# Optimization experiments

Hardware: AMD Instinct MI355X
Metric: run time of the kernel (lower is better)

## Reference

```python
import jax, jax.numpy as jnp
import numpy as np

C = 1.0          # ball curvature (k = -1/c with c=1.0 in the torch module)
SQC = 1.0        # sqrt(C)
LN_EPS = 1e-5

def _artanh(x):
    return jnp.arctanh(jnp.clip(x, -1.0 + 1e-7, 1.0 - 1e-7))

def _norm(x):
    # last-dim L2 norm, clamped away from zero for stable division
    return jnp.clip(jnp.sqrt(jnp.sum(x * x, axis=-1, keepdims=True)), 1e-7, None)

def expmap0(u):
    un = _norm(u)
    return jnp.tanh(SQC * un) * u / (SQC * un)

def logmap0(y):
    yn = _norm(y)
    return _artanh(SQC * yn) * y / (SQC * yn)

def mobius_add(x, y):
    x2 = jnp.sum(x * x, axis=-1, keepdims=True)
    y2 = jnp.sum(y * y, axis=-1, keepdims=True)
    xy = jnp.sum(x * y, axis=-1, keepdims=True)
    num = (1.0 + 2.0 * C * xy + C * y2) * x + (1.0 - C * x2) * y
    den = 1.0 + 2.0 * C * xy + C * C * x2 * y2
    return num / jnp.clip(den, 1e-15, None)

def mobius_matvec(W, x):
    # W: [H, D], x: [B, D] -> [B, H]
    mx = x @ W.T
    xn = _norm(x)
    mxn = _norm(mx)
    res = jnp.tanh(mxn / xn * _artanh(SQC * xn)) * mx / (SQC * mxn)
    return jnp.where(mxn <= 1e-7, jnp.zeros_like(res), res)

def mobius_pointwise_mul(w, x):
    wx = w * x
    xn = _norm(x)
    wxn = _norm(wx)
    res = jnp.tanh(wxn / xn * _artanh(SQC * xn)) * wx / (SQC * wxn)
    return jnp.where(wxn <= 1e-7, jnp.zeros_like(res), res)

def layer_norm(x, g, b):
    mu = jnp.mean(x, axis=-1, keepdims=True)
    var = jnp.mean((x - mu) ** 2, axis=-1, keepdims=True)
    return (x - mu) * jax.lax.rsqrt(var + LN_EPS) * g + b

def one_rnn_transform(W, h, U, x, b):
    Wh = mobius_matvec(W, h)
    Ux = mobius_matvec(U, x)
    return mobius_add(mobius_add(Wh, Ux), b)

def setup_inputs() -> dict:
    key = jax.random.key(0)
    B, I, H = 65536, 256, 256
    k1, k2, k3, k4, k5 = jax.random.split(key, 5)
    stdv = 1.0 / np.sqrt(H)
    # points on the Poincare ball via expmap0 of small tangent vectors
    x = expmap0(0.02 * jax.random.normal(k1, (B, I), dtype=jnp.float32))
    hx = expmap0(0.02 * jax.random.normal(k2, (B, H), dtype=jnp.float32))
    weight_ih = jax.random.uniform(k3, (3 * H, I), dtype=jnp.float32, minval=-stdv, maxval=stdv)
    weight_hh = jax.random.uniform(k4, (3 * H, H), dtype=jnp.float32, minval=-stdv, maxval=stdv)
    bias = 0.01 * jax.random.normal(k5, (3, H), dtype=jnp.float32)
    ln_gamma = jnp.ones((3, H), dtype=jnp.float32)
    ln_beta = jnp.zeros((3, H), dtype=jnp.float32)
    return {"input": x, "hx": hx, "weight_ih": weight_ih, "weight_hh": weight_hh,
            "bias": bias, "ln_gamma": ln_gamma, "ln_beta": ln_beta}

def reference(input, hx, weight_ih, weight_hh, bias, ln_gamma, ln_beta):
    H = hx.shape[-1]
    W_ir, W_ih_, W_iz = weight_ih[:H], weight_ih[H:2*H], weight_ih[2*H:]
    W_hr, W_hh_, W_hz = weight_hh[:H], weight_hh[H:2*H], weight_hh[2*H:]
    b_r, b_h, b_z = bias[0], bias[1], bias[2]
    temp_z = logmap0(one_rnn_transform(W_hz, hx, W_iz, input, b_z))
    temp_r = logmap0(one_rnn_transform(W_hr, hx, W_ir, input, b_r))
    z_t = jax.nn.sigmoid(layer_norm(temp_z, ln_gamma[0], ln_beta[0]))
    r_t = jax.nn.sigmoid(layer_norm(temp_r, ln_gamma[1], ln_beta[1]))
    rh_t = mobius_pointwise_mul(r_t, hx)
    h_tilde = one_rnn_transform(W_hh_, rh_t, W_ih_, input, b_h)
    h_tilde = expmap0(jnp.tanh(layer_norm(logmap0(h_tilde), ln_gamma[2], ln_beta[2])))
    temp_1 = mobius_pointwise_mul(1.0 - z_t, hx)
    temp_2 = mobius_pointwise_mul(z_t, h_tilde)
    return mobius_add(temp_1, temp_2)
```

## Files before the change

kernel.cpp:

```cpp
#include <hip/hip_runtime.h>
#include <math.h>

#define HD  256
#define BM  16
#define NTH 256

typedef __attribute__((ext_vector_type(8))) short bf16x8;
typedef __attribute__((ext_vector_type(4))) float f32x4;

__device__ __forceinline__ float rcp_f(float x){ return __builtin_amdgcn_rcpf(x); }
__device__ __forceinline__ float tanh_f(float x){
  float ax = fabsf(x);
  float e  = __expf(-2.f*ax);
  float t  = (1.f - e) * rcp_f(1.f + e);
  return copysignf(t, x);
}
__device__ __forceinline__ float artanh_f(float v){
  v = fminf(fmaxf(v, -1.f + 1e-7f), 1.f - 1e-7f);
  return 0.5f * __logf((1.f + v) * rcp_f(1.f - v));
}
__device__ __forceinline__ float sigmoid_f(float v){ return rcp_f(1.f + __expf(-v)); }
__device__ __forceinline__ unsigned short f2bf(float f){
  unsigned u = __float_as_uint(f);
  u += 0x7FFFu + ((u >> 16) & 1u);
  return (unsigned short)(u >> 16);
}
__device__ __forceinline__ float bf2f(unsigned short h){
  return __uint_as_float(((unsigned)h) << 16);
}
__device__ __forceinline__ int swz(int R, int C){
  return R*HD + (((C >> 3) ^ (R & 7)) << 3) + (C & 7);
}

__global__ void convert_w_kernel(const float* __restrict__ Wih,
                                 const float* __restrict__ Whh,
                                 unsigned short* __restrict__ wb){
  int c = blockIdx.x * blockDim.x + threadIdx.x;
  if (c >= 6 * 8192) return;
  int mat = c >> 13;
  int ci  = c & 8191;
  int l = ci & 63, st = ci >> 6;
  int s = st & 7, ct = st >> 3;
  int col = ct * 16 + (l & 15);
  int k0  = s * 32 + (l >> 4) * 8;
  const float* src = (mat < 3) ? (Wih + (size_t)mat * HD * HD)
                               : (Whh + (size_t)(mat - 3) * HD * HD);
  const float* p = src + (size_t)col * HD + k0;
  unsigned short tmp[8];
  #pragma unroll
  for (int j = 0; j < 8; ++j) tmp[j] = f2bf(p[j]);
  *(bf16x8*)(wb + (size_t)mat * 65536 + (size_t)ci * 8) = *(bf16x8*)tmp;
}

__device__ __forceinline__ void gate_gemm(
    const unsigned short* ldsH, const unsigned short* __restrict__ wH,
    const unsigned short* ldsX, const unsigned short* __restrict__ wX,
    f32x4 A[4], f32x4 Bx[4], int wc, int lr, int lg, int l){
  #pragma unroll
  for (int n = 0; n < 4; ++n){
    A[n]  = (f32x4){0.f,0.f,0.f,0.f};
    Bx[n] = (f32x4){0.f,0.f,0.f,0.f};
  }
  #pragma unroll
  for (int s = 0; s < 8; ++s){
    int idx = lr*HD + (((4*s + lg) ^ (lr & 7)) << 3);
    bf16x8 ah = *(const bf16x8*)&ldsH[idx];
    bf16x8 ax = *(const bf16x8*)&ldsX[idx];
    #pragma unroll
    for (int n = 0; n < 4; ++n){
      int ct = wc*4 + n;
      int off = ((ct*8 + s)*64 + l)*8;
      bf16x8 bh = *(const bf16x8*)(wH + off);
      bf16x8 bx = *(const bf16x8*)(wX + off);
      A[n]  = __builtin_amdgcn_mfma_f32_16x16x32_bf16(ah, bh, A[n], 0, 0, 0);
      Bx[n] = __builtin_amdgcn_mfma_f32_16x16x32_bf16(ax, bx, Bx[n], 0, 0, 0);
    }
  }
}

__device__ __forceinline__ void gate_reduce_chain(
    const f32x4 (&A)[4], const f32x4 (&Bx)[4], const float (&bt)[4],
    float (*RED)[33], float (*kco)[9], float (*srow)[BM], const float* sbb,
    int rowA, int gidx, int t, int wc, int lr, int lg){
  float p[7][4];
  #pragma unroll
  for (int q = 0; q < 4; ++q){
    float a2=0.f,b2=0.f,ab=0.f,sA=0.f,sB=0.f,Ab=0.f,Bb=0.f;
    #pragma unroll
    for (int n = 0; n < 4; ++n){
      float ae = A[n][q], be = Bx[n][q], bv = bt[n];
      a2 = fmaf(ae,ae,a2); b2 = fmaf(be,be,b2); ab = fmaf(ae,be,ab);
      sA += ae; sB += be; Ab = fmaf(ae,bv,Ab); Bb = fmaf(be,bv,Bb);
    }
    p[0][q]=a2; p[1][q]=b2; p[2][q]=ab; p[3][q]=sA; p[4][q]=sB; p[5][q]=Ab; p[6][q]=Bb;
  }
  #pragma unroll
  for (int j = 0; j < 7; ++j)
    #pragma unroll
    for (int q = 0; q < 4; ++q){
      float v = p[j][q];
      v += __shfl_xor(v,1); v += __shfl_xor(v,2);
      v += __shfl_xor(v,4); v += __shfl_xor(v,8);
      p[j][q] = v;
    }
  if (lr == 0){
    #pragma unroll
    for (int q = 0; q < 4; ++q){
      int R = lg*4 + q;
      #pragma unroll
      for (int j = 0; j < 7; ++j) RED[R][wc*8 + j] = p[j][q];
    }
  }
  __syncthreads();
  if (t < BM){
    int R = t;
    float s[7];
    #pragma unroll
    for (int j = 0; j < 7; ++j)
      s[j] = RED[R][j] + RED[R][8+j] + RED[R][16+j] + RED[R][24+j];
    float bb  = sbb[gidx];
    float sbs = sbb[4+gidx];
    float an = srow[rowA][R], aa = srow[rowA+1][R];
    float bn = srow[0][R],    ba = srow[1][R];
    float mraw = sqrtf(s[0]); float mA = fmaxf(mraw, 1e-7f);
    float tA = tanh_f(mA / an * aa);
    float sa  = (mraw <= 1e-7f) ? 0.f : tA / mA;
    float x2a = (mraw <= 1e-7f) ? 0.f : tA*tA;
    float nraw = sqrtf(s[1]); float mB = fmaxf(nraw, 1e-7f);
    float tB = tanh_f(mB / bn * ba);
    float sb_ = (nraw <= 1e-7f) ? 0.f : tB / mB;
    float x2b = (nraw <= 1e-7f) ? 0.f : tB*tB;
    float xy = sa*sb_*s[2];
    float ca = 1.f + 2.f*xy + x2b;
    float cb = 1.f - x2a;
    float den = fmaxf(1.f + 2.f*xy + x2a*x2b, 1e-15f);
    float u = ca*sa/den, v = cb*sb_/den;
    float P2 = u*u*s[0] + 2.f*u*v*s[2] + v*v*s[1];
    float Pb = u*s[5] + v*s[6];
    float sP = u*s[3] + v*s[4];
    float ca2 = 1.f + 2.f*Pb + bb;
    float cb2 = 1.f - P2;
    float den2 = fmaxf(1.f + 2.f*Pb + P2*bb, 1e-15f);
    float pp = ca2/den2, ww = cb2/den2;
    float Q2 = pp*pp*P2 + 2.f*pp*ww*Pb + ww*ww*bb;
    float sQsum = pp*sP + ww*sbs;
    float qn = fmaxf(sqrtf(Q2), 1e-7f);
    float sQ = artanh_f(qn) / qn;
    float mu = sQ*sQsum*(1.f/HD);
    float e2 = sQ*sQ*Q2*(1.f/HD);
    float is = rsqrtf(e2 - mu*mu + 1e-5f);
    kco[R][0] = sQ*pp*u;  kco[R][1] = sQ*pp*v;  kco[R][2] = sQ*ww;
    kco[R][3] = mu;       kco[R][4] = is;
  }
  __syncthreads();
}

__global__ __launch_bounds__(NTH, 2) void mobius_gru_mfma(
    const float* __restrict__ x, const float* __restrict__ hx,
    const unsigned short* __restrict__ wbih, const unsigned short* __restrict__ wbhh,
    const float* __restrict__ bias, const float* __restrict__ gam,
    const float* __restrict__ bet, float* __restrict__ out, int B){
  __shared__ unsigned short xb[BM*HD];
  __shared__ unsigned short hb[BM*HD];
  __shared__ float RED[BM][33];
  __shared__ float kco[BM][9];
  __shared__ float srow[8][BM];
  __shared__ float sbb[8];

  const int t  = threadIdx.x;
  const int l  = t & 63;
  const int lr = l & 15, lg = l >> 4;
  const int wc = t >> 6;
  const size_t row0 = (size_t)blockIdx.x * BM;

  {
    float* spart = &RED[0][0];
    int r = t >> 4, seg = t & 15;
    const float* xp = x  + (row0 + r)*HD + seg*16;
    const float* hp = hx + (row0 + r)*HD + seg*16;
    float sx = 0.f, sh = 0.f;
    #pragma unroll
    for (int i = 0; i < 4; ++i){
      int c = seg*16 + i*4;
      int di = swz(r, c);
      float4 v = *(const float4*)(xp + i*4);
      sx += v.x*v.x + v.y*v.y + v.z*v.z + v.w*v.w;
      ushort4 o = { f2bf(v.x), f2bf(v.y), f2bf(v.z), f2bf(v.w) };
      *(ushort4*)&xb[di] = o;
      v = *(const float4*)(hp + i*4);
      sh += v.x*v.x + v.y*v.y + v.z*v.z + v.w*v.w;
      ushort4 o2 = { f2bf(v.x), f2bf(v.y), f2bf(v.z), f2bf(v.w) };
      *(ushort4*)&hb[di] = o2;
    }
    spart[r*16 + seg] = sx; spart[256 + r*16 + seg] = sh;
  }
  if (t >= 64 && t < 256){
    int g = (t >> 6) - 1;
    float4 b4 = *(const float4*)&bias[g*HD + (t & 63)*4];
    float p2 = b4.x*b4.x + b4.y*b4.y + b4.z*b4.z + b4.w*b4.w;
    float ps = b4.x + b4.y + b4.z + b4.w;
    #pragma unroll
    for (int m = 1; m <= 32; m <<= 1){ p2 += __shfl_xor(p2, m); ps += __shfl_xor(ps, m); }
    if ((t & 63) == 0){ sbb[g] = p2; sbb[4+g] = ps; }
  }
  __syncthreads();
  if (t < BM){
    float* spart = &RED[0][0];
    float sx = 0.f, sh = 0.f;
    #pragma unroll
    for (int i = 0; i < 16; ++i){ sx += spart[t*16 + i]; sh += spart[256 + t*16 + i]; }
    float xn = fmaxf(sqrtf(sx), 1e-7f);
    float hn = fmaxf(sqrtf(sh), 1e-7f);
    srow[0][t] = xn; srow[1][t] = artanh_f(xn);
    srow[2][t] = hn; srow[3][t] = artanh_f(hn);
  }
  __syncthreads();

  f32x4 A[4], Bx[4];
  float bt[4], gv[4], bv[4];
  unsigned ztp[4][2];
  float hvreg[4][4];

  #pragma unroll
  for (int n = 0; n < 4; ++n){
    int C = wc*64 + n*16 + lr;
    bt[n] = bias[2*HD + C]; gv[n] = gam[C]; bv[n] = bet[C];
  }
  gate_gemm(hb, wbhh + 2*65536, xb, wbih + 2*65536, A, Bx, wc, lr, lg, l);
  gate_reduce_chain(A, Bx, bt, RED, kco, srow, sbb, 2, 2, t, wc, lr, lg);
  #pragma unroll
  for (int q = 0; q < 4; ++q){
    int R = lg*4 + q;
    float KA=kco[R][0], KB=kco[R][1], Kb=kco[R][2], mu=kco[R][3], is=kco[R][4];
    #pragma unroll
    for (int n = 0; n < 4; ++n){
      float ln = (KA*A[n][q] + KB*Bx[n][q] + Kb*bt[n] - mu)*is*gv[n] + bv[n];
      unsigned zb = f2bf(sigmoid_f(ln));
      if ((q & 1) == 0) ztp[n][q>>1] = zb;
      else              ztp[n][q>>1] |= (zb << 16);
    }
  }

  #pragma unroll
  for (int n = 0; n < 4; ++n){
    int C = wc*64 + n*16 + lr;
    bt[n] = bias[C]; gv[n] = gam[HD + C]; bv[n] = bet[HD + C];
  }
  gate_gemm(hb, wbhh, xb, wbih, A, Bx, wc, lr, lg, l);
  gate_reduce_chain(A, Bx, bt, RED, kco, srow, sbb, 2, 0, t, wc, lr, lg);
  {
    #pragma unroll
    for (int q = 0; q < 4; ++q){
      int R = lg*4 + q;
      float KA=kco[R][0], KB=kco[R][1], Kb=kco[R][2], mu=kco[R][3], is=kco[R][4];
      float acc = 0.f;
      #pragma unroll
      for (int n = 0; n < 4; ++n){
        int C = wc*64 + n*16 + lr;
        float hv = bf2f(hb[swz(R, C)]);
        hvreg[n][q] = hv;
        float ln = (KA*A[n][q] + KB*Bx[n][q] + Kb*bt[n] - mu)*is*gv[n] + bv[n];
        float rhv = sigmoid_f(ln) * hv;
        Bx[n][q] = rhv;
        acc = fmaf(rhv, rhv, acc);
      }
      float v2 = acc;
      v2 += __shfl_xor(v2,1); v2 += __shfl_xor(v2,2);
      v2 += __shfl_xor(v2,4); v2 += __shfl_xor(v2,8);
      if (lr == 0) RED[R][wc*8] = v2;
    }
  }
  __syncthreads();
  if (t < BM){
    int R = t;
    float s0 = RED[R][0] + RED[R][8] + RED[R][16] + RED[R][24];
    float wraw = sqrtf(s0); float wn = fmaxf(wraw, 1e-7f);
    float s = tanh_f(wn / srow[2][R] * srow[3][R]);
    float sc = (wraw <= 1e-7f) ? 0.f : s / wn;
    float rn = fmaxf((wraw <= 1e-7f) ? 0.f : fabsf(s), 1e-7f);
    kco[R][0] = sc; srow[4][R] = rn; srow[5][R] = artanh_f(rn);
  }
  __syncthreads();
  #pragma unroll
  for (int q = 0; q < 4; ++q){
    int R = lg*4 + q;
    float sc = kco[R][0];
    #pragma unroll
    for (int n = 0; n < 4; ++n){
      int C = wc*64 + n*16 + lr;
      hb[swz(R, C)] = f2bf(sc * Bx[n][q]);
    }
  }
  __syncthreads();

  #pragma unroll
  for (int n = 0; n < 4; ++n){
    int C = wc*64 + n*16 + lr;
    bt[n] = bias[HD + C]; gv[n] = gam[2*HD + C]; bv[n] = bet[2*HD + C];
  }
  gate_gemm(hb, wbhh + 65536, xb, wbih + 65536, A, Bx, wc, lr, lg, l);
  gate_reduce_chain(A, Bx, bt, RED, kco, srow, sbb, 4, 1, t, wc, lr, lg);
  {
    #pragma unroll
    for (int q = 0; q < 4; ++q){
      int R = lg*4 + q;
      float KA=kco[R][0], KB=kco[R][1], Kb=kco[R][2], mu=kco[R][3], is=kco[R][4];
      float acc = 0.f;
      #pragma unroll
      for (int n = 0; n < 4; ++n){
        float ln = (KA*A[n][q] + KB*Bx[n][q] + Kb*bt[n] - mu)*is*gv[n] + bv[n];
        float uv = tanh_f(ln);
        A[n][q] = uv;
        acc = fmaf(uv, uv, acc);
      }
      float v2 = acc;
      v2 += __shfl_xor(v2,1); v2 += __shfl_xor(v2,2);
      v2 += __shfl_xor(v2,4); v2 += __shfl_xor(v2,8);
      if (lr == 0) RED[R][wc*8] = v2;
    }
  }
  __syncthreads();
  if (t < BM){
    int R = t;
    float s0 = RED[R][0] + RED[R][8] + RED[R][16] + RED[R][24];
    float unraw = sqrtf(s0);
    float un = fmaxf(unraw, 1e-7f);
    float es = tanh_f(un) / un;
    float htn = fmaxf(es * unraw, 1e-7f);
    kco[R][0] = es; srow[6][R] = htn; srow[7][R] = artanh_f(htn);
  }
  __syncthreads();

  #pragma unroll
  for (int q = 0; q < 4; ++q){
    int R = lg*4 + q;
    float es = kco[R][0];
    float a1 = 0.f, a2 = 0.f, a12 = 0.f;
    #pragma unroll
    for (int n = 0; n < 4; ++n){
      unsigned zp = ztp[n][q >> 1];
      float zv = __uint_as_float((q & 1) ? (zp & 0xFFFF0000u) : (zp << 16));
      float w2v = zv * es * A[n][q];
      float w1v = (1.f - zv) * hvreg[n][q];
      A[n][q]  = w1v;
      Bx[n][q] = w2v;
      a1 = fmaf(w1v, w1v, a1); a2 = fmaf(w2v, w2v, a2); a12 = fmaf(w1v, w2v, a12);
    }
    float v1 = a1, v2 = a2, v3 = a12;
    v1 += __shfl_xor(v1,1); v2 += __shfl_xor(v2,1); v3 += __shfl_xor(v3,1);
    v1 += __shfl_xor(v1,2); v2 += __shfl_xor(v2,2); v3 += __shfl_xor(v3,2);
    v1 += __shfl_xor(v1,4); v2 += __shfl_xor(v2,4); v3 += __shfl_xor(v3,4);
    v1 += __shfl_xor(v1,8); v2 += __shfl_xor(v2,8); v3 += __shfl_xor(v3,8);
    if (lr == 0){
      RED[R][wc*8]   = v1;
      RED[R][wc*8+1] = v2;
      RED[R][wc*8+2] = v3;
    }
  }
  __syncthreads();
  if (t < BM){
    int R = t;
    float s1  = RED[R][0] + RED[R][8]  + RED[R][16] + RED[R][24];
    float s2  = RED[R][1] + RED[R][9]  + RED[R][17] + RED[R][25];
    float s12 = RED[R][2] + RED[R][10] + RED[R][18] + RED[R][26];
    float raw1 = sqrtf(s1); float n1 = fmaxf(raw1, 1e-7f);
    float ss1 = tanh_f(n1 / srow[2][R] * srow[3][R]);
    float sc1 = (raw1 <= 1e-7f) ? 0.f : ss1 / n1;
    float t1  = (raw1 <= 1e-7f) ? 0.f : ss1*ss1;
    float raw2 = sqrtf(s2); float n2 = fmaxf(raw2, 1e-7f);
    float ss2 = tanh_f(n2 / srow[6][R] * srow[7][R]);
    float sc2 = (raw2 <= 1e-7f) ? 0.f : ss2 / n2;
    float t2  = (raw2 <= 1e-7f) ? 0.f : ss2*ss2;
    float xy = sc1*sc2*s12;
    float ca = 1.f + 2.f*xy + t2;
    float cb = 1.f - t1;
    float den = fmaxf(1.f + 2.f*xy + t1*t2, 1e-15f);
    kco[R][0] = ca*sc1/den;
    kco[R][1] = cb*sc2/den;
  }
  __syncthreads();
  #pragma unroll
  for (int q = 0; q < 4; ++q){
    int R = lg*4 + q;
    float cw1 = kco[R][0], cw2 = kco[R][1];
    #pragma unroll
    for (int n = 0; n < 4; ++n){
      int C = wc*64 + n*16 + lr;
      out[(row0 + R)*HD + C] = cw1*A[n][q] + cw2*Bx[n][q];
    }
  }
}

extern "C" void kernel_launch(void* const* d_in, const int* in_sizes, int n_in,
                              void* d_out, int out_size, void* d_ws, size_t ws_size,
                              hipStream_t stream){
  const float* x    = (const float*)d_in[0];
  const float* hx   = (const float*)d_in[1];
  const float* Wih  = (const float*)d_in[2];
  const float* Whh  = (const float*)d_in[3];
  const float* bias = (const float*)d_in[4];
  const float* gam  = (const float*)d_in[5];
  const float* bet  = (const float*)d_in[6];
  float* out = (float*)d_out;
  unsigned short* wb = (unsigned short*)d_ws;
  const int B = in_sizes[0] / HD;

  hipLaunchKernelGGL(convert_w_kernel, dim3(192), dim3(256), 0, stream, Wih, Whh, wb);
  hipLaunchKernelGGL(mobius_gru_mfma, dim3(B / BM), dim3(NTH), 0, stream,
                     x, hx, wb, wb + 3*65536, bias, gam, bet, out, B);
}
```

Measured before the change: 222.8 us.

## Process 32 rows per block so each weight fragment feeds two MFMA row groups

Raises the block's row tile from 16 to 32. Each bf16 weight fragment fetched from global memory now feeds two 16-row MFMA accumulator sets, which halves weight traffic per output row. All per-row epilogue loops (reductions, gate math, stores) gain an outer loop over the two row groups, and the input staging is remapped to 8 threads per row. The cost is roughly double the accumulator and per-thread state registers, which may lower occupancy, and half as many blocks in the grid.

```diff
diff --git a/kernel.cpp b/kernel.cpp
--- a/kernel.cpp
+++ b/kernel.cpp
@@ -2,7 +2,7 @@
 #include <math.h>
 
 #define HD  256
-#define BM  16
+#define BM  32
 #define NTH 256
 
 typedef __attribute__((ext_vector_type(8))) short bf16x8;
@@ -55,60 +55,71 @@
 __device__ __forceinline__ void gate_gemm(
     const unsigned short* ldsH, const unsigned short* __restrict__ wH,
     const unsigned short* ldsX, const unsigned short* __restrict__ wX,
-    f32x4 A[4], f32x4 Bx[4], int wc, int lr, int lg, int l){
-  #pragma unroll
-  for (int n = 0; n < 4; ++n){
-    A[n]  = (f32x4){0.f,0.f,0.f,0.f};
-    Bx[n] = (f32x4){0.f,0.f,0.f,0.f};
-  }
+    f32x4 A[2][4], f32x4 Bx[2][4], int wc, int lr, int lg, int l){
+  #pragma unroll
+  for (int g = 0; g < 2; ++g)
+    #pragma unroll
+    for (int n = 0; n < 4; ++n){
+      A[g][n]  = (f32x4){0.f,0.f,0.f,0.f};
+      Bx[g][n] = (f32x4){0.f,0.f,0.f,0.f};
+    }
   #pragma unroll
   for (int s = 0; s < 8; ++s){
-    int idx = lr*HD + (((4*s + lg) ^ (lr & 7)) << 3);
-    bf16x8 ah = *(const bf16x8*)&ldsH[idx];
-    bf16x8 ax = *(const bf16x8*)&ldsX[idx];
+    int col = (((4*s + lg) ^ (lr & 7)) << 3);
+    int i0 = lr*HD + col;
+    int i1 = (lr + 16)*HD + col;
+    bf16x8 ah0 = *(const bf16x8*)&ldsH[i0];
+    bf16x8 ah1 = *(const bf16x8*)&ldsH[i1];
+    bf16x8 ax0 = *(const bf16x8*)&ldsX[i0];
+    bf16x8 ax1 = *(const bf16x8*)&ldsX[i1];
     #pragma unroll
     for (int n = 0; n < 4; ++n){
       int ct = wc*4 + n;
       int off = ((ct*8 + s)*64 + l)*8;
       bf16x8 bh = *(const bf16x8*)(wH + off);
       bf16x8 bx = *(const bf16x8*)(wX + off);
-      A[n]  = __builtin_amdgcn_mfma_f32_16x16x32_bf16(ah, bh, A[n], 0, 0, 0);
-      Bx[n] = __builtin_amdgcn_mfma_f32_16x16x32_bf16(ax, bx, Bx[n], 0, 0, 0);
+      A[0][n]  = __builtin_amdgcn_mfma_f32_16x16x32_bf16(ah0, bh, A[0][n], 0, 0, 0);
+      A[1][n]  = __builtin_amdgcn_mfma_f32_16x16x32_bf16(ah1, bh, A[1][n], 0, 0, 0);
+      Bx[0][n] = __builtin_amdgcn_mfma_f32_16x16x32_bf16(ax0, bx, Bx[0][n], 0, 0, 0);
+      Bx[1][n] = __builtin_amdgcn_mfma_f32_16x16x32_bf16(ax1, bx, Bx[1][n], 0, 0, 0);
     }
   }
 }
 
 __device__ __forceinline__ void gate_reduce_chain(
-    const f32x4 (&A)[4], const f32x4 (&Bx)[4], const float (&bt)[4],
+    const f32x4 (&A)[2][4], const f32x4 (&Bx)[2][4], const float (&bt)[4],
     float (*RED)[33], float (*kco)[9], float (*srow)[BM], const float* sbb,
     int rowA, int gidx, int t, int wc, int lr, int lg){
-  float p[7][4];
-  #pragma unroll
-  for (int q = 0; q < 4; ++q){
-    float a2=0.f,b2=0.f,ab=0.f,sA=0.f,sB=0.f,Ab=0.f,Bb=0.f;
-    #pragma unroll
-    for (int n = 0; n < 4; ++n){
-      float ae = A[n][q], be = Bx[n][q], bv = bt[n];
-      a2 = fmaf(ae,ae,a2); b2 = fmaf(be,be,b2); ab = fmaf(ae,be,ab);
-      sA += ae; sB += be; Ab = fmaf(ae,bv,Ab); Bb = fmaf(be,bv,Bb);
-    }
-    p[0][q]=a2; p[1][q]=b2; p[2][q]=ab; p[3][q]=sA; p[4][q]=sB; p[5][q]=Ab; p[6][q]=Bb;
-  }
-  #pragma unroll
-  for (int j = 0; j < 7; ++j)
+  #pragma unroll
+  for (int g = 0; g < 2; ++g){
+    float p[7][4];
     #pragma unroll
     for (int q = 0; q < 4; ++q){
-      float v = p[j][q];
-      v += __shfl_xor(v,1); v += __shfl_xor(v,2);
-      v += __shfl_xor(v,4); v += __shfl_xor(v,8);
-      p[j][q] = v;
-    }
-  if (lr == 0){
-    #pragma unroll
-    for (int q = 0; q < 4; ++q){
-      int R = lg*4 + q;
-      #pragma unroll
-      for (int j = 0; j < 7; ++j) RED[R][wc*8 + j] = p[j][q];
+      float a2=0.f,b2=0.f,ab=0.f,sA=0.f,sB=0.f,Ab=0.f,Bb=0.f;
+      #pragma unroll
+      for (int n = 0; n < 4; ++n){
+        float ae = A[g][n][q], be = Bx[g][n][q], bv = bt[n];
+        a2 = fmaf(ae,ae,a2); b2 = fmaf(be,be,b2); ab = fmaf(ae,be,ab);
+        sA += ae; sB += be; Ab = fmaf(ae,bv,Ab); Bb = fmaf(be,bv,Bb);
+      }
+      p[0][q]=a2; p[1][q]=b2; p[2][q]=ab; p[3][q]=sA; p[4][q]=sB; p[5][q]=Ab; p[6][q]=Bb;
+    }
+    #pragma unroll
+    for (int j = 0; j < 7; ++j)
+      #pragma unroll
+      for (int q = 0; q < 4; ++q){
+        float v = p[j][q];
+        v += __shfl_xor(v,1); v += __shfl_xor(v,2);
+        v += __shfl_xor(v,4); v += __shfl_xor(v,8);
+        p[j][q] = v;
+      }
+    if (lr == 0){
+      #pragma unroll
+      for (int q = 0; q < 4; ++q){
+        int R = g*16 + lg*4 + q;
+        #pragma unroll
+        for (int j = 0; j < 7; ++j) RED[R][wc*8 + j] = p[j][q];
+      }
     }
   }
   __syncthreads();
@@ -175,13 +186,13 @@
 
   {
     float* spart = &RED[0][0];
-    int r = t >> 4, seg = t & 15;
-    const float* xp = x  + (row0 + r)*HD + seg*16;
-    const float* hp = hx + (row0 + r)*HD + seg*16;
+    int r = t >> 3, seg = t & 7;
+    const float* xp = x  + (row0 + r)*HD + seg*32;
+    const float* hp = hx + (row0 + r)*HD + seg*32;
     float sx = 0.f, sh = 0.f;
     #pragma unroll
-    for (int i = 0; i < 4; ++i){
-      int c = seg*16 + i*4;
+    for (int i = 0; i < 8; ++i){
+      int c = seg*32 + i*4;
       int di = swz(r, c);
       float4 v = *(const float4*)(xp + i*4);
       sx += v.x*v.x + v.y*v.y + v.z*v.z + v.w*v.w;
@@ -192,7 +203,7 @@
       ushort4 o2 = { f2bf(v.x), f2bf(v.y), f2bf(v.z), f2bf(v.w) };
       *(ushort4*)&hb[di] = o2;
     }
-    spart[r*16 + seg] = sx; spart[256 + r*16 + seg] = sh;
+    spart[r*8 + seg] = sx; spart[256 + r*8 + seg] = sh;
   }
   if (t >= 64 && t < 256){
     int g = (t >> 6) - 1;
@@ -208,7 +219,7 @@
     float* spart = &RED[0][0];
     float sx = 0.f, sh = 0.f;
     #pragma unroll
-    for (int i = 0; i < 16; ++i){ sx += spart[t*16 + i]; sh += spart[256 + t*16 + i]; }
+    for (int i = 0; i < 8; ++i){ sx += spart[t*8 + i]; sh += spart[256 + t*8 + i]; }
     float xn = fmaxf(sqrtf(sx), 1e-7f);
     float hn = fmaxf(sqrtf(sh), 1e-7f);
     srow[0][t] = xn; srow[1][t] = artanh_f(xn);
@@ -216,10 +227,10 @@
   }
   __syncthreads();
 
-  f32x4 A[4], Bx[4];
+  f32x4 A[2][4], Bx[2][4];
   float bt[4], gv[4], bv[4];
-  unsigned ztp[4][2];
-  float hvreg[4][4];
+  unsigned ztp[2][4][2];
+  float hvreg[2][4][4];
 
   #pragma unroll
   for (int n = 0; n < 4; ++n){
@@ -229,17 +240,19 @@
   gate_gemm(hb, wbhh + 2*65536, xb, wbih + 2*65536, A, Bx, wc, lr, lg, l);
   gate_reduce_chain(A, Bx, bt, RED, kco, srow, sbb, 2, 2, t, wc, lr, lg);
   #pragma unroll
-  for (int q = 0; q < 4; ++q){
-    int R = lg*4 + q;
-    float KA=kco[R][0], KB=kco[R][1], Kb=kco[R][2], mu=kco[R][3], is=kco[R][4];
-    #pragma unroll
-    for (int n = 0; n < 4; ++n){
-      float ln = (KA*A[n][q] + KB*Bx[n][q] + Kb*bt[n] - mu)*is*gv[n] + bv[n];
-      unsigned zb = f2bf(sigmoid_f(ln));
-      if ((q & 1) == 0) ztp[n][q>>1] = zb;
-      else              ztp[n][q>>1] |= (zb << 16);
-    }
-  }
+  for (int g = 0; g < 2; ++g)
+    #pragma unroll
+    for (int q = 0; q < 4; ++q){
+      int R = g*16 + lg*4 + q;
+      float KA=kco[R][0], KB=kco[R][1], Kb=kco[R][2], mu=kco[R][3], is=kco[R][4];
+      #pragma unroll
+      for (int n = 0; n < 4; ++n){
+        float ln = (KA*A[g][n][q] + KB*Bx[g][n][q] + Kb*bt[n] - mu)*is*gv[n] + bv[n];
+        unsigned zb = f2bf(sigmoid_f(ln));
+        if ((q & 1) == 0) ztp[g][n][q>>1] = zb;
+        else              ztp[g][n][q>>1] |= (zb << 16);
+      }
+    }
 
   #pragma unroll
   for (int n = 0; n < 4; ++n){
@@ -250,25 +263,27 @@
   gate_reduce_chain(A, Bx, bt, RED, kco, srow, sbb, 2, 0, t, wc, lr, lg);
   {
     #pragma unroll
-    for (int q = 0; q < 4; ++q){
-      int R = lg*4 + q;
-      float KA=kco[R][0], KB=kco[R][1], Kb=kco[R][2], mu=kco[R][3], is=kco[R][4];
-      float acc = 0.f;
-      #pragma unroll
-      for (int n = 0; n < 4; ++n){
-        int C = wc*64 + n*16 + lr;
-        float hv = bf2f(hb[swz(R, C)]);
-        hvreg[n][q] = hv;
-        float ln = (KA*A[n][q] + KB*Bx[n][q] + Kb*bt[n] - mu)*is*gv[n] + bv[n];
-        float rhv = sigmoid_f(ln) * hv;
-        Bx[n][q] = rhv;
-        acc = fmaf(rhv, rhv, acc);
-      }
-      float v2 = acc;
-      v2 += __shfl_xor(v2,1); v2 += __shfl_xor(v2,2);
-      v2 += __shfl_xor(v2,4); v2 += __shfl_xor(v2,8);
-      if (lr == 0) RED[R][wc*8] = v2;
-    }
+    for (int g = 0; g < 2; ++g)
+      #pragma unroll
+      for (int q = 0; q < 4; ++q){
+        int R = g*16 + lg*4 + q;
+        float KA=kco[R][0], KB=kco[R][1], Kb=kco[R][2], mu=kco[R][3], is=kco[R][4];
+        float acc = 0.f;
+        #pragma unroll
+        for (int n = 0; n < 4; ++n){
+          int C = wc*64 + n*16 + lr;
+          float hv = bf2f(hb[swz(R, C)]);
+          hvreg[g][n][q] = hv;
+          float ln = (KA*A[g][n][q] + KB*Bx[g][n][q] + Kb*bt[n] - mu)*is*gv[n] + bv[n];
+          float rhv = sigmoid_f(ln) * hv;
+          Bx[g][n][q] = rhv;
+          acc = fmaf(rhv, rhv, acc);
+        }
+        float v2 = acc;
+        v2 += __shfl_xor(v2,1); v2 += __shfl_xor(v2,2);
+        v2 += __shfl_xor(v2,4); v2 += __shfl_xor(v2,8);
+        if (lr == 0) RED[R][wc*8] = v2;
+      }
   }
   __syncthreads();
   if (t < BM){
@@ -282,15 +297,17 @@
   }
   __syncthreads();
   #pragma unroll
-  for (int q = 0; q < 4; ++q){
-    int R = lg*4 + q;
-    float sc = kco[R][0];
-    #pragma unroll
-    for (int n = 0; n < 4; ++n){
-      int C = wc*64 + n*16 + lr;
-      hb[swz(R, C)] = f2bf(sc * Bx[n][q]);
-    }
-  }
+  for (int g = 0; g < 2; ++g)
+    #pragma unroll
+    for (int q = 0; q < 4; ++q){
+      int R = g*16 + lg*4 + q;
+      float sc = kco[R][0];
+      #pragma unroll
+      for (int n = 0; n < 4; ++n){
+        int C = wc*64 + n*16 + lr;
+        hb[swz(R, C)] = f2bf(sc * Bx[g][n][q]);
+      }
+    }
   __syncthreads();
 
   #pragma unroll
@@ -302,22 +319,24 @@
   gate_reduce_chain(A, Bx, bt, RED, kco, srow, sbb, 4, 1, t, wc, lr, lg);
   {
     #pragma unroll
-    for (int q = 0; q < 4; ++q){
-      int R = lg*4 + q;
-      float KA=kco[R][0], KB=kco[R][1], Kb=kco[R][2], mu=kco[R][3], is=kco[R][4];
-      float acc = 0.f;
-      #pragma unroll
-      for (int n = 0; n < 4; ++n){
-        float ln = (KA*A[n][q] + KB*Bx[n][q] + Kb*bt[n] - mu)*is*gv[n] + bv[n];
-        float uv = tanh_f(ln);
-        A[n][q] = uv;
-        acc = fmaf(uv, uv, acc);
-      }
-      float v2 = acc;
-      v2 += __shfl_xor(v2,1); v2 += __shfl_xor(v2,2);
-      v2 += __shfl_xor(v2,4); v2 += __shfl_xor(v2,8);
-      if (lr == 0) RED[R][wc*8] = v2;
-    }
+    for (int g = 0; g < 2; ++g)
+      #pragma unroll
+      for (int q = 0; q < 4; ++q){
+        int R = g*16 + lg*4 + q;
+        float KA=kco[R][0], KB=kco[R][1], Kb=kco[R][2], mu=kco[R][3], is=kco[R][4];
+        float acc = 0.f;
+        #pragma unroll
+        for (int n = 0; n < 4; ++n){
+          float ln = (KA*A[g][n][q] + KB*Bx[g][n][q] + Kb*bt[n] - mu)*is*gv[n] + bv[n];
+          float uv = tanh_f(ln);
+          A[g][n][q] = uv;
+          acc = fmaf(uv, uv, acc);
+        }
+        float v2 = acc;
+        v2 += __shfl_xor(v2,1); v2 += __shfl_xor(v2,2);
+        v2 += __shfl_xor(v2,4); v2 += __shfl_xor(v2,8);
+        if (lr == 0) RED[R][wc*8] = v2;
+      }
   }
   __syncthreads();
   if (t < BM){
@@ -332,31 +351,33 @@
   __syncthreads();
 
   #pragma unroll
-  for (int q = 0; q < 4; ++q){
-    int R = lg*4 + q;
-    float es = kco[R][0];
-    float a1 = 0.f, a2 = 0.f, a12 = 0.f;
-    #pragma unroll
-    for (int n = 0; n < 4; ++n){
-      unsigned zp = ztp[n][q >> 1];
-      float zv = __uint_as_float((q & 1) ? (zp & 0xFFFF0000u) : (zp << 16));
-      float w2v = zv * es * A[n][q];
-      float w1v = (1.f - zv) * hvreg[n][q];
-      A[n][q]  = w1v;
-      Bx[n][q] = w2v;
-      a1 = fmaf(w1v, w1v, a1); a2 = fmaf(w2v, w2v, a2); a12 = fmaf(w1v, w2v, a12);
-    }
-    float v1 = a1, v2 = a2, v3 = a12;
-    v1 += __shfl_xor(v1,1); v2 += __shfl_xor(v2,1); v3 += __shfl_xor(v3,1);
-    v1 += __shfl_xor(v1,2); v2 += __shfl_xor(v2,2); v3 += __shfl_xor(v3,2);
-    v1 += __shfl_xor(v1,4); v2 += __shfl_xor(v2,4); v3 += __shfl_xor(v3,4);
-    v1 += __shfl_xor(v1,8); v2 += __shfl_xor(v2,8); v3 += __shfl_xor(v3,8);
-    if (lr == 0){
-      RED[R][wc*8]   = v1;
-      RED[R][wc*8+1] = v2;
-      RED[R][wc*8+2] = v3;
-    }
-  }
+  for (int g = 0; g < 2; ++g)
+    #pragma unroll
+    for (int q = 0; q < 4; ++q){
+      int R = g*16 + lg*4 + q;
+      float es = kco[R][0];
+      float a1 = 0.f, a2 = 0.f, a12 = 0.f;
+      #pragma unroll
+      for (int n = 0; n < 4; ++n){
+        unsigned zp = ztp[g][n][q >> 1];
+        float zv = __uint_as_float((q & 1) ? (zp & 0xFFFF0000u) : (zp << 16));
+        float w2v = zv * es * A[g][n][q];
+        float w1v = (1.f - zv) * hvreg[g][n][q];
+        A[g][n][q]  = w1v;
+        Bx[g][n][q] = w2v;
+        a1 = fmaf(w1v, w1v, a1); a2 = fmaf(w2v, w2v, a2); a12 = fmaf(w1v, w2v, a12);
+      }
+      float v1 = a1, v2 = a2, v3 = a12;
+      v1 += __shfl_xor(v1,1); v2 += __shfl_xor(v2,1); v3 += __shfl_xor(v3,1);
+      v1 += __shfl_xor(v1,2); v2 += __shfl_xor(v2,2); v3 += __shfl_xor(v3,2);
+      v1 += __shfl_xor(v1,4); v2 += __shfl_xor(v2,4); v3 += __shfl_xor(v3,4);
+      v1 += __shfl_xor(v1,8); v2 += __shfl_xor(v2,8); v3 += __shfl_xor(v3,8);
+      if (lr == 0){
+        RED[R][wc*8]   = v1;
+        RED[R][wc*8+1] = v2;
+        RED[R][wc*8+2] = v3;
+      }
+    }
   __syncthreads();
   if (t < BM){
     int R = t;
@@ -380,15 +401,17 @@
   }
   __syncthreads();
   #pragma unroll
-  for (int q = 0; q < 4; ++q){
-    int R = lg*4 + q;
-    float cw1 = kco[R][0], cw2 = kco[R][1];
-    #pragma unroll
-    for (int n = 0; n < 4; ++n){
-      int C = wc*64 + n*16 + lr;
-      out[(row0 + R)*HD + C] = cw1*A[n][q] + cw2*Bx[n][q];
-    }
-  }
+  for (int g = 0; g < 2; ++g)
+    #pragma unroll
+    for (int q = 0; q < 4; ++q){
+      int R = g*16 + lg*4 + q;
+      float cw1 = kco[R][0], cw2 = kco[R][1];
+      #pragma unroll
+      for (int n = 0; n < 4; ++n){
+        int C = wc*64 + n*16 + lr;
+        out[(row0 + R)*HD + C] = cw1*A[g][n][q] + cw2*Bx[g][n][q];
+      }
+    }
 }
 
 extern "C" void kernel_launch(void* const* d_in, const int* in_sizes, int n_in,
```

New measurement: 293.6 us. +31.8%, slower.

## Split each row tile across eight waves instead of four

Applied to the files above, without the earlier changes.

Doubles the block to 512 threads (8 waves), so each wave computes two 16-column MFMA tiles per gate instead of four. The per-row reductions in shared memory grow to eight partial slots, and the launch bound asks for 4 blocks per CU. The goal is more waves in flight to hide the latency of the global weight loads and the serial per-row epilogue chains. The cost is more cross-wave reduction work and barriers spread over more threads, plus tighter per-thread register limits.

```diff
diff --git a/kernel.cpp b/kernel.cpp
--- a/kernel.cpp
+++ b/kernel.cpp
@@ -3,7 +3,8 @@
 
 #define HD  256
 #define BM  16
-#define NTH 256
+#define NTH 512
+#define NW  8
 
 typedef __attribute__((ext_vector_type(8))) short bf16x8;
 typedef __attribute__((ext_vector_type(4))) float f32x4;
@@ -55,9 +56,9 @@
 __device__ __forceinline__ void gate_gemm(
     const unsigned short* ldsH, const unsigned short* __restrict__ wH,
     const unsigned short* ldsX, const unsigned short* __restrict__ wX,
-    f32x4 A[4], f32x4 Bx[4], int wc, int lr, int lg, int l){
-  #pragma unroll
-  for (int n = 0; n < 4; ++n){
+    f32x4 A[2], f32x4 Bx[2], int wc, int lr, int lg, int l){
+  #pragma unroll
+  for (int n = 0; n < 2; ++n){
     A[n]  = (f32x4){0.f,0.f,0.f,0.f};
     Bx[n] = (f32x4){0.f,0.f,0.f,0.f};
   }
@@ -67,8 +68,8 @@
     bf16x8 ah = *(const bf16x8*)&ldsH[idx];
     bf16x8 ax = *(const bf16x8*)&ldsX[idx];
     #pragma unroll
-    for (int n = 0; n < 4; ++n){
-      int ct = wc*4 + n;
+    for (int n = 0; n < 2; ++n){
+      int ct = wc*2 + n;
       int off = ((ct*8 + s)*64 + l)*8;
       bf16x8 bh = *(const bf16x8*)(wH + off);
       bf16x8 bx = *(const bf16x8*)(wX + off);
@@ -79,15 +80,15 @@
 }
 
 __device__ __forceinline__ void gate_reduce_chain(
-    const f32x4 (&A)[4], const f32x4 (&Bx)[4], const float (&bt)[4],
-    float (*RED)[33], float (*kco)[9], float (*srow)[BM], const float* sbb,
+    const f32x4 (&A)[2], const f32x4 (&Bx)[2], const float (&bt)[2],
+    float (*RED)[57], float (*kco)[9], float (*srow)[BM], const float* sbb,
     int rowA, int gidx, int t, int wc, int lr, int lg){
   float p[7][4];
   #pragma unroll
   for (int q = 0; q < 4; ++q){
     float a2=0.f,b2=0.f,ab=0.f,sA=0.f,sB=0.f,Ab=0.f,Bb=0.f;
     #pragma unroll
-    for (int n = 0; n < 4; ++n){
+    for (int n = 0; n < 2; ++n){
       float ae = A[n][q], be = Bx[n][q], bv = bt[n];
       a2 = fmaf(ae,ae,a2); b2 = fmaf(be,be,b2); ab = fmaf(ae,be,ab);
       sA += ae; sB += be; Ab = fmaf(ae,bv,Ab); Bb = fmaf(be,bv,Bb);
@@ -108,7 +109,7 @@
     for (int q = 0; q < 4; ++q){
       int R = lg*4 + q;
       #pragma unroll
-      for (int j = 0; j < 7; ++j) RED[R][wc*8 + j] = p[j][q];
+      for (int j = 0; j < 7; ++j) RED[R][wc*7 + j] = p[j][q];
     }
   }
   __syncthreads();
@@ -116,8 +117,12 @@
     int R = t;
     float s[7];
     #pragma unroll
-    for (int j = 0; j < 7; ++j)
-      s[j] = RED[R][j] + RED[R][8+j] + RED[R][16+j] + RED[R][24+j];
+    for (int j = 0; j < 7; ++j){
+      float acc = 0.f;
+      #pragma unroll
+      for (int w = 0; w < NW; ++w) acc += RED[R][w*7 + j];
+      s[j] = acc;
+    }
     float bb  = sbb[gidx];
     float sbs = sbb[4+gidx];
     float an = srow[rowA][R], aa = srow[rowA+1][R];
@@ -155,14 +160,15 @@
   __syncthreads();
 }
 
-__global__ __launch_bounds__(NTH, 2) void mobius_gru_mfma(
+__global__ __launch_bounds__(NTH, 4) void mobius_gru_mfma(
     const float* __restrict__ x, const float* __restrict__ hx,
     const unsigned short* __restrict__ wbih, const unsigned short* __restrict__ wbhh,
     const float* __restrict__ bias, const float* __restrict__ gam,
     const float* __restrict__ bet, float* __restrict__ out, int B){
   __shared__ unsigned short xb[BM*HD];
   __shared__ unsigned short hb[BM*HD];
-  __shared__ float RED[BM][33];
+  __shared__ float spart[2*NTH];
+  __shared__ float RED[BM][57];
   __shared__ float kco[BM][9];
   __shared__ float srow[8][BM];
   __shared__ float sbb[8];
@@ -174,14 +180,13 @@
   const size_t row0 = (size_t)blockIdx.x * BM;
 
   {
-    float* spart = &RED[0][0];
-    int r = t >> 4, seg = t & 15;
-    const float* xp = x  + (row0 + r)*HD + seg*16;
-    const float* hp = hx + (row0 + r)*HD + seg*16;
+    int r = t >> 5, seg = t & 31;
+    const float* xp = x  + (row0 + r)*HD + seg*8;
+    const float* hp = hx + (row0 + r)*HD + seg*8;
     float sx = 0.f, sh = 0.f;
     #pragma unroll
-    for (int i = 0; i < 4; ++i){
-      int c = seg*16 + i*4;
+    for (int i = 0; i < 2; ++i){
+      int c = seg*8 + i*4;
       int di = swz(r, c);
       float4 v = *(const float4*)(xp + i*4);
       sx += v.x*v.x + v.y*v.y + v.z*v.z + v.w*v.w;
@@ -192,7 +197,7 @@
       ushort4 o2 = { f2bf(v.x), f2bf(v.y), f2bf(v.z), f2bf(v.w) };
       *(ushort4*)&hb[di] = o2;
     }
-    spart[r*16 + seg] = sx; spart[256 + r*16 + seg] = sh;
+    spart[t] = sx; spart[NTH + t] = sh;
   }
   if (t >= 64 && t < 256){
     int g = (t >> 6) - 1;
@@ -205,10 +210,9 @@
   }
   __syncthreads();
   if (t < BM){
-    float* spart = &RED[0][0];
     float sx = 0.f, sh = 0.f;
     #pragma unroll
-    for (int i = 0; i < 16; ++i){ sx += spart[t*16 + i]; sh += spart[256 + t*16 + i]; }
+    for (int i = 0; i < 32; ++i){ sx += spart[t*32 + i]; sh += spart[NTH + t*32 + i]; }
     float xn = fmaxf(sqrtf(sx), 1e-7f);
     float hn = fmaxf(sqrtf(sh), 1e-7f);
     srow[0][t] = xn; srow[1][t] = artanh_f(xn);
@@ -216,14 +220,14 @@
   }
   __syncthreads();
 
-  f32x4 A[4], Bx[4];
-  float bt[4], gv[4], bv[4];
-  unsigned ztp[4][2];
-  float hvreg[4][4];
-
-  #pragma unroll
-  for (int n = 0; n < 4; ++n){
-    int C = wc*64 + n*16 + lr;
+  f32x4 A[2], Bx[2];
+  float bt[2], gv[2], bv[2];
+  unsigned ztp[2][2];
+  float hvreg[2][4];
+
+  #pragma unroll
+  for (int n = 0; n < 2; ++n){
+    int C = wc*32 + n*16 + lr;
     bt[n] = bias[2*HD + C]; gv[n] = gam[C]; bv[n] = bet[C];
   }
   gate_gemm(hb, wbhh + 2*65536, xb, wbih + 2*65536, A, Bx, wc, lr, lg, l);
@@ -233,7 +237,7 @@
     int R = lg*4 + q;
     float KA=kco[R][0], KB=kco[R][1], Kb=kco[R][2], mu=kco[R][3], is=kco[R][4];
     #pragma unroll
-    for (int n = 0; n < 4; ++n){
+    for (int n = 0; n < 2; ++n){
       float ln = (KA*A[n][q] + KB*Bx[n][q] + Kb*bt[n] - mu)*is*gv[n] + bv[n];
       unsigned zb = f2bf(sigmoid_f(ln));
       if ((q & 1) == 0) ztp[n][q>>1] = zb;
@@ -242,8 +246,8 @@
   }
 
   #pragma unroll
-  for (int n = 0; n < 4; ++n){
-    int C = wc*64 + n*16 + lr;
+  for (int n = 0; n < 2; ++n){
+    int C = wc*32 + n*16 + lr;
     bt[n] = bias[C]; gv[n] = gam[HD + C]; bv[n] = bet[HD + C];
   }
   gate_gemm(hb, wbhh, xb, wbih, A, Bx, wc, lr, lg, l);
@@ -255,8 +259,8 @@
       float KA=kco[R][0], KB=kco[R][1], Kb=kco[R][2], mu=kco[R][3], is=kco[R][4];
       float acc = 0.f;
       #pragma unroll
-      for (int n = 0; n < 4; ++n){
-        int C = wc*64 + n*16 + lr;
+      for (int n = 0; n < 2; ++n){
+        int C = wc*32 + n*16 + lr;
         float hv = bf2f(hb[swz(R, C)]);
         hvreg[n][q] = hv;
         float ln = (KA*A[n][q] + KB*Bx[n][q] + Kb*bt[n] - mu)*is*gv[n] + bv[n];
@@ -267,13 +271,15 @@
       float v2 = acc;
       v2 += __shfl_xor(v2,1); v2 += __shfl_xor(v2,2);
       v2 += __shfl_xor(v2,4); v2 += __shfl_xor(v2,8);
-      if (lr == 0) RED[R][wc*8] = v2;
+      if (lr == 0) RED[R][wc*7] = v2;
     }
   }
   __syncthreads();
   if (t < BM){
     int R = t;
-    float s0 = RED[R][0] + RED[R][8] + RED[R][16] + RED[R][24];
+    float s0 = 0.f;
+    #pragma unroll
+    for (int w = 0; w < NW; ++w) s0 += RED[R][w*7];
     float wraw = sqrtf(s0); float wn = fmaxf(wraw, 1e-7f);
     float s = tanh_f(wn / srow[2][R] * srow[3][R]);
     float sc = (wraw <= 1e-7f) ? 0.f : s / wn;
@@ -286,16 +292,16 @@
     int R = lg*4 + q;
     float sc = kco[R][0];
     #pragma unroll
-    for (int n = 0; n < 4; ++n){
-      int C = wc*64 + n*16 + lr;
+    for (int n = 0; n < 2; ++n){
+      int C = wc*32 + n*16 + lr;
       hb[swz(R, C)] = f2bf(sc * Bx[n][q]);
     }
   }
   __syncthreads();
 
   #pragma unroll
-  for (int n = 0; n < 4; ++n){
-    int C = wc*64 + n*16 + lr;
+  for (int n = 0; n < 2; ++n){
+    int C = wc*32 + n*16 + lr;
     bt[n] = bias[HD + C]; gv[n] = gam[2*HD + C]; bv[n] = bet[2*HD + C];
   }
   gate_gemm(hb, wbhh + 65536, xb, wbih + 65536, A, Bx, wc, lr, lg, l);
@@ -307,7 +313,7 @@
       float KA=kco[R][0], KB=kco[R][1], Kb=kco[R][2], mu=kco[R][3], is=kco[R][4];
       float acc = 0.f;
       #pragma unroll
-      for (int n = 0; n < 4; ++n){
+      for (int n = 0; n < 2; ++n){
         float ln = (KA*A[n][q] + KB*Bx[n][q] + Kb*bt[n] - mu)*is*gv[n] + bv[n];
         float uv = tanh_f(ln);
         A[n][q] = uv;
@@ -316,13 +322,15 @@
       float v2 = acc;
       v2 += __shfl_xor(v2,1); v2 += __shfl_xor(v2,2);
       v2 += __shfl_xor(v2,4); v2 += __shfl_xor(v2,8);
-      if (lr == 0) RED[R][wc*8] = v2;
+      if (lr == 0) RED[R][wc*7] = v2;
     }
   }
   __syncthreads();
   if (t < BM){
     int R = t;
-    float s0 = RED[R][0] + RED[R][8] + RED[R][16] + RED[R][24];
+    float s0 = 0.f;
+    #pragma unroll
+    for (int w = 0; w < NW; ++w) s0 += RED[R][w*7];
     float unraw = sqrtf(s0);
     float un = fmaxf(unraw, 1e-7f);
     float es = tanh_f(un) / un;
@@ -337,7 +345,7 @@
     float es = kco[R][0];
     float a1 = 0.f, a2 = 0.f, a12 = 0.f;
     #pragma unroll
-    for (int n = 0; n < 4; ++n){
+    for (int n = 0; n < 2; ++n){
       unsigned zp = ztp[n][q >> 1];
       float zv = __uint_as_float((q & 1) ? (zp & 0xFFFF0000u) : (zp << 16));
       float w2v = zv * es * A[n][q];
@@ -352,17 +360,19 @@
     v1 += __shfl_xor(v1,4); v2 += __shfl_xor(v2,4); v3 += __shfl_xor(v3,4);
     v1 += __shfl_xor(v1,8); v2 += __shfl_xor(v2,8); v3 += __shfl_xor(v3,8);
     if (lr == 0){
-      RED[R][wc*8]   = v1;
-      RED[R][wc*8+1] = v2;
-      RED[R][wc*8+2] = v3;
+      RED[R][wc*7]   = v1;
+      RED[R][wc*7+1] = v2;
+      RED[R][wc*7+2] = v3;
     }
   }
   __syncthreads();
   if (t < BM){
     int R = t;
-    float s1  = RED[R][0] + RED[R][8]  + RED[R][16] + RED[R][24];
-    float s2  = RED[R][1] + RED[R][9]  + RED[R][17] + RED[R][25];
-    float s12 = RED[R][2] + RED[R][10] + RED[R][18] + RED[R][26];
+    float s1 = 0.f, s2 = 0.f, s12 = 0.f;
+    #pragma unroll
+    for (int w = 0; w < NW; ++w){
+      s1 += RED[R][w*7]; s2 += RED[R][w*7+1]; s12 += RED[R][w*7+2];
+    }
     float raw1 = sqrtf(s1); float n1 = fmaxf(raw1, 1e-7f);
     float ss1 = tanh_f(n1 / srow[2][R] * srow[3][R]);
     float sc1 = (raw1 <= 1e-7f) ? 0.f : ss1 / n1;
@@ -384,8 +394,8 @@
     int R = lg*4 + q;
     float cw1 = kco[R][0], cw2 = kco[R][1];
     #pragma unroll
-    for (int n = 0; n < 4; ++n){
-      int C = wc*64 + n*16 + lr;
+    for (int n = 0; n < 2; ++n){
+      int C = wc*32 + n*16 + lr;
       out[(row0 + R)*HD + C] = cw1*A[n][q] + cw2*Bx[n][q];
     }
   }
```

Result: slower. 329.3 us (+47.8%).
